# Kernel tuning notes

Hardware: AMD Instinct MI355X
Metric: run time of the kernel (lower is better)

The kernel has to match this reference:

```python
import jax, jax.numpy as jnp
import numpy as np

B, S, N, U, A = 256, 24, 207, 64, 256
H = N * U  # hidden_state_size = num_nodes * rnn_units


def setup_inputs() -> dict:
    key = jax.random.key(0)
    ks = jax.random.split(key, 9)
    return {
        "inputs": jax.random.normal(ks[0], (B, N), dtype=jnp.float32),
        "encoder_outputs": jax.random.normal(ks[1], (S, B, H), dtype=jnp.float32),
        "hidden_state": jax.random.normal(ks[2], (1, B, H), dtype=jnp.float32) * 0.05,
        "adj": jax.random.uniform(ks[3], (N, N), dtype=jnp.float32) / N,
        "attn_W": jax.random.normal(ks[4], (2 * H, A), dtype=jnp.float32) * 0.01,
        "attn_b": jnp.zeros((A,), dtype=jnp.float32),
        "attn_v": jax.random.normal(ks[5], (A,), dtype=jnp.float32) * 0.1,
        "W_ru": jax.random.normal(ks[6], (1 + 2 * U, 2 * U), dtype=jnp.float32) * 0.1,
        "b_ru": jnp.zeros((2 * U,), dtype=jnp.float32),
        "W_c": jax.random.normal(ks[7], (1 + 2 * U, U), dtype=jnp.float32) * 0.1,
        "b_c": jnp.zeros((U,), dtype=jnp.float32),
        "proj_W": jax.random.normal(ks[8], (2 * U + 1, 1), dtype=jnp.float32) * 0.1,
        "proj_b": jnp.zeros((1,), dtype=jnp.float32),
    }


def reference(inputs, encoder_outputs, hidden_state, adj, attn_W, attn_b, attn_v,
              W_ru, b_ru, W_c, b_c, proj_W, proj_b):
    b = inputs.shape[0]
    hid = hidden_state[-1]                               # (B, H) top-layer decoder state
    enc = jnp.transpose(encoder_outputs, (1, 0, 2))      # (B, S, H)

    # Bahdanau attention: tanh(Linear(cat(hid, enc))) . v, softmax over src_len.
    # Split the weight so we never materialize the (B, S, 2H) concat.
    Wh, We = attn_W[:H], attn_W[H:]
    energy = jnp.tanh((hid @ Wh)[:, None, :] + jnp.einsum('bsh,ha->bsa', enc, We) + attn_b)
    scores = energy @ attn_v                             # (B, S)
    a = jax.nn.softmax(scores, axis=1)
    weighted = jnp.einsum('bs,bsh->bh', a, enc).reshape(b, N, U)  # (B, N, U)

    # Graph-conv GRU cell (DCRNN-style), single layer.
    x = jnp.concatenate([inputs.reshape(b, N, 1), weighted], axis=-1)  # (B, N, 1+U)
    h = hid.reshape(b, N, U)
    m = jnp.einsum('nm,bmf->bnf', adj, jnp.concatenate([x, h], axis=-1))  # message passing
    ru = jax.nn.sigmoid(m @ W_ru + b_ru)                 # (B, N, 2U)
    r, u = ru[..., :U], ru[..., U:]
    mc = jnp.einsum('nm,bmf->bnf', adj, jnp.concatenate([x, r * h], axis=-1))
    c = jnp.tanh(mc @ W_c + b_c)                         # (B, N, U)
    new_h = u * h + (1.0 - u) * c                        # (B, N, U)

    # Projection: Linear(2U+1 -> 1) on per-node cat(output, weighted, inputs).
    proj_in = jnp.concatenate([new_h, weighted, inputs.reshape(b, N, 1)], axis=-1)
    output = (proj_in @ proj_W + proj_b).reshape(b, N)   # (B, N*output_dim)
    return output, new_h.reshape(1, b, H)
```

## Files before the change

### kernel.cpp

```cpp
#include <hip/hip_runtime.h>
#include <hip/hip_bf16.h>
#include <math.h>

#define B_ 256
#define S_ 24
#define N_ 207
#define U_ 64
#define A_ 256
#define H_ (N_*U_)
#define H2_ (2*H_)
#define BS_ (B_*S_)
#define NF_ 129
#define FP_ 192
#define KP_ 256

typedef __attribute__((ext_vector_type(8))) short bf16x8;
typedef __attribute__((ext_vector_type(4))) float f32x4;

#define GAS __attribute__((address_space(1)))
#define LAS __attribute__((address_space(3)))

static __device__ __forceinline__ void gload16(const __hip_bfloat16* g, void* lds) {
    __builtin_amdgcn_global_load_lds((const GAS uint32_t*)g, (LAS uint32_t*)lds, 16, 0, 0);
}

template<int BM, int BN, int EPI>
__global__ __launch_bounds__(256)
void mfma_gemm(const __hip_bfloat16* __restrict__ A, int lda,
               const __hip_bfloat16* __restrict__ BT, int ldb,
               void* __restrict__ Cv, int ldc,
               int kchunk, int niter,
               const float* __restrict__ ep0,
               const float* __restrict__ ep1,
               const float* __restrict__ ep2)
{
    constexpr int FM = BM / 32, FN = BN / 32;
    __shared__ __align__(128) char smem[(BM + BN) * 128];
    char* As = smem;
    char* Bs = smem + BM * 128;

    const int tid  = threadIdx.x;
    const int lane = tid & 63;
    const int wid  = tid >> 6;
    const int wr   = wid >> 1, wc = wid & 1;

    const int n0 = blockIdx.x * BN;
    const int m0 = blockIdx.y * BM;
    const long k0 = (long)blockIdx.z * kchunk;

    const int qk = lane >> 4;
    const int fr = lane & 15;
    const int sw = (lane & 7) << 4;

    f32x4 acc[FM][FN] = {};

    for (int it = 0; it < niter; ++it) {
        const long kb = k0 + (long)it * 64;
        #pragma unroll
        for (int p = 0; p < BM / 32; ++p) {
            const int chunk = p * 4 + wid;
            const int blk   = chunk * 64 + lane;
            const int r     = blk >> 3;
            const int klog  = ((blk & 7) << 4) ^ ((r & 7) << 4);
            gload16(A + (size_t)(m0 + r) * lda + kb + (klog >> 1), As + chunk * 1024);
        }
        #pragma unroll
        for (int p = 0; p < BN / 32; ++p) {
            const int chunk = p * 4 + wid;
            const int blk   = chunk * 64 + lane;
            const int r     = blk >> 3;
            const int klog  = ((blk & 7) << 4) ^ ((r & 7) << 4);
            gload16(BT + (size_t)(n0 + r) * ldb + kb + (klog >> 1), Bs + chunk * 1024);
        }
        __syncthreads();
        #pragma unroll
        for (int ks = 0; ks < 2; ++ks) {
            const int ko = ks * 64 + qk * 16;
            bf16x8 a[FM], b[FN];
            #pragma unroll
            for (int i = 0; i < FM; ++i)
                a[i] = *(const bf16x8*)(As + (wr * (BM/2) + i * 16 + fr) * 128 + (ko ^ sw));
            #pragma unroll
            for (int j = 0; j < FN; ++j)
                b[j] = *(const bf16x8*)(Bs + (wc * (BN/2) + j * 16 + fr) * 128 + (ko ^ sw));
            #pragma unroll
            for (int i = 0; i < FM; ++i)
                #pragma unroll
                for (int j = 0; j < FN; ++j)
                    acc[i][j] = __builtin_amdgcn_mfma_f32_16x16x32_bf16(a[i], b[j], acc[i][j], 0, 0, 0);
        }
        __syncthreads();
    }

    #pragma unroll
    for (int mi = 0; mi < FM; ++mi)
        #pragma unroll
        for (int ni = 0; ni < FN; ++ni) {
            const int rbase = m0 + wr * (BM/2) + mi * 16 + qk * 4;
            const int col   = n0 + wc * (BN/2) + ni * 16 + fr;
            #pragma unroll
            for (int q = 0; q < 4; ++q) {
                const int row = rbase + q;
                const float v = acc[mi][ni][q];
                if (EPI == 1) {
                    atomicAdd(&((float*)Cv)[(size_t)row * ldc + col], v);
                } else if (EPI == 2) {
                    ((__hip_bfloat16*)Cv)[(size_t)row * ldc + col] = __float2bfloat16(v);
                } else if (EPI == 3) {
                    const int bb = col >> 6, uu = col & 63;
                    ((__hip_bfloat16*)Cv)[((size_t)row * 256 + bb) * FP_ + 65 + uu] = __float2bfloat16(v);
                } else if (EPI == 4) {
                    float sv = v + ep0[col];
                    ((float*)Cv)[(size_t)row * ldc + col] = 1.f / (1.f + expf(-sv));
                } else {
                    const int nn = row >> 8, bb = row & 255;
                    float cg = tanhf(v + ep0[col]);
                    float ug = ep1[(size_t)row * 128 + 64 + col];
                    float hh = ep2[(size_t)bb * H_ + nn * U_ + col];
                    ((float*)Cv)[(size_t)bb * H_ + nn * U_ + col] = ug * hh + (1.f - ug) * cg;
                }
            }
        }
}

__global__ __launch_bounds__(256)
void gemm_enchid(const float* __restrict__ Aenc,
                 const float* __restrict__ Ahid,
                 const __hip_bfloat16* __restrict__ WTBF,
                 float* __restrict__ P, float* __restrict__ T1,
                 int kchunk, int niter)
{
    __shared__ __align__(128) char smem[(64 + 256) * 128];
    char* As = smem;
    char* Bs = smem + 64*128;

    const int tid  = threadIdx.x;
    const int lane = tid & 63;
    const int wid  = tid >> 6;
    const int wr   = wid >> 1, wc = wid & 1;

    const bool isH = (blockIdx.y >= 96);
    const float* A = isH ? Ahid : Aenc;
    const int m0   = (isH ? (blockIdx.y - 96) : blockIdx.y) * 64;
    const __hip_bfloat16* BT = WTBF + (isH ? 0 : H_);
    float* C = isH ? T1 : P;

    const long k0 = (long)blockIdx.z * kchunk;

    const int qk = lane >> 4;
    const int fr = lane & 15;
    const int sw = (lane & 7) << 4;

    f32x4 acc[2][8] = {};

    for (int it = 0; it < niter; ++it) {
        const long kb = k0 + (long)it * 64;
        #pragma unroll
        for (int h = 0; h < 2; ++h) {
            const int c  = h * 256 + tid;
            const int r  = c >> 3;
            const int kc = c & 7;
            const float* src = A + (size_t)(m0 + r) * H_ + kb + kc * 8;
            const float4 x = *(const float4*)(src);
            const float4 y = *(const float4*)(src + 4);
            union { __hip_bfloat16 hh[8]; int4 u; } pk;
            pk.hh[0] = __float2bfloat16(x.x); pk.hh[1] = __float2bfloat16(x.y);
            pk.hh[2] = __float2bfloat16(x.z); pk.hh[3] = __float2bfloat16(x.w);
            pk.hh[4] = __float2bfloat16(y.x); pk.hh[5] = __float2bfloat16(y.y);
            pk.hh[6] = __float2bfloat16(y.z); pk.hh[7] = __float2bfloat16(y.w);
            *(int4*)(As + r * 128 + ((kc << 4) ^ ((r & 7) << 4))) = pk.u;
        }
        #pragma unroll
        for (int p = 0; p < 8; ++p) {
            const int chunk = p * 4 + wid;
            const int blk   = chunk * 64 + lane;
            const int r     = blk >> 3;
            const int klog  = ((blk & 7) << 4) ^ ((r & 7) << 4);
            gload16(BT + (size_t)r * H2_ + kb + (klog >> 1), Bs + chunk * 1024);
        }
        __syncthreads();
        #pragma unroll
        for (int ks = 0; ks < 2; ++ks) {
            const int ko = ks * 64 + qk * 16;
            bf16x8 a[2], b[8];
            #pragma unroll
            for (int i = 0; i < 2; ++i)
                a[i] = *(const bf16x8*)(As + (wr * 32 + i * 16 + fr) * 128 + (ko ^ sw));
            #pragma unroll
            for (int j = 0; j < 8; ++j)
                b[j] = *(const bf16x8*)(Bs + (wc * 128 + j * 16 + fr) * 128 + (ko ^ sw));
            #pragma unroll
            for (int i = 0; i < 2; ++i)
                #pragma unroll
                for (int j = 0; j < 8; ++j)
                    acc[i][j] = __builtin_amdgcn_mfma_f32_16x16x32_bf16(a[i], b[j], acc[i][j], 0, 0, 0);
        }
        __syncthreads();
    }

    #pragma unroll
    for (int mi = 0; mi < 2; ++mi)
        #pragma unroll
        for (int ni = 0; ni < 8; ++ni) {
            const int rbase = m0 + wr * 32 + mi * 16 + qk * 4;
            const int col   = wc * 128 + ni * 16 + fr;
            #pragma unroll
            for (int q = 0; q < 4; ++q)
                atomicAdd(&C[(size_t)(rbase + q) * A_ + col], acc[mi][ni][q]);
        }
}

__global__ __launch_bounds__(256)
void init_kernel(const float* __restrict__ ab, float* __restrict__ T1,
                 float4* __restrict__ P4) {
    int i = blockIdx.x * 256 + threadIdx.x;
    if (blockIdx.x < 256) {
        T1[i] = ab[i & 255];
    } else {
        P4[i - 65536] = make_float4(0.f, 0.f, 0.f, 0.f);
    }
}

__global__ __launch_bounds__(256)
void transpose_cvt_kernel(const float* __restrict__ in, __hip_bfloat16* __restrict__ out) {
    __shared__ float tile[32][33];
    const int h0 = blockIdx.x * 32, a0 = blockIdx.y * 32;
    const int tx = threadIdx.x & 31, ty4 = threadIdx.x >> 5;
    #pragma unroll
    for (int i = 0; i < 4; ++i) {
        int r = ty4 * 4 + i;
        tile[r][tx] = in[(size_t)(h0 + r) * A_ + a0 + tx];
    }
    __syncthreads();
    #pragma unroll
    for (int i = 0; i < 4; ++i) {
        int r = ty4 * 4 + i;
        out[(size_t)(a0 + r) * H2_ + h0 + tx] = __float2bfloat16(tile[tx][r]);
    }
}

__global__ __launch_bounds__(256)
void scores_kernel(const float* __restrict__ P, const float* __restrict__ T1,
                   const float* __restrict__ v, float* __restrict__ SC) {
    int wave = threadIdx.x >> 6, lane = threadIdx.x & 63;
    int q = blockIdx.x * 4 + wave;
    if (q >= BS_) return;
    int b = q & 255;
    float s = 0.f;
    #pragma unroll
    for (int a = lane; a < A_; a += 64) {
        float e = tanhf(P[(size_t)q * A_ + a] + T1[b * A_ + a]);
        s += e * v[a];
    }
    #pragma unroll
    for (int off = 32; off; off >>= 1) s += __shfl_down(s, off, 64);
    if (lane == 0) SC[q] = s;
}

__global__ __launch_bounds__(256)
void weighted_f32_kernel(const float4* __restrict__ E4, const float* __restrict__ SC,
                         float4* __restrict__ WT4) {
    int g = blockIdx.x * 256 + threadIdx.x;
    int b = g / (H_ / 4), c = g % (H_ / 4);
    float sc[S_];
    float mx = -1e30f;
    #pragma unroll
    for (int s = 0; s < S_; ++s) { sc[s] = SC[s * B_ + b]; mx = fmaxf(mx, sc[s]); }
    float sum = 0.f;
    #pragma unroll
    for (int s = 0; s < S_; ++s) { sc[s] = expf(sc[s] - mx); sum += sc[s]; }
    float inv = 1.f / sum;
    float4 acc = make_float4(0.f, 0.f, 0.f, 0.f);
    #pragma unroll
    for (int s = 0; s < S_; ++s) {
        float w = sc[s] * inv;
        float4 ev = E4[(size_t)(s * B_ + b) * (H_ / 4) + c];
        acc.x += w * ev.x; acc.y += w * ev.y;
        acc.z += w * ev.z; acc.w += w * ev.w;
    }
    WT4[(size_t)b * (H_ / 4) + c] = acc;
}

__global__ __launch_bounds__(256)
void catT_prepB_kernel(const float* __restrict__ inp, const float* __restrict__ WT,
                       const float* __restrict__ hid, __hip_bfloat16* __restrict__ CT,
                       const float* __restrict__ adj, const float* __restrict__ Wru,
                       const float* __restrict__ Wc, __hip_bfloat16* __restrict__ ADJ,
                       __hip_bfloat16* __restrict__ WRUT, __hip_bfloat16* __restrict__ WCT) {
    const int tid = threadIdx.x;
    if (blockIdx.y == 4) {
        for (int i = blockIdx.x * 256 + tid; i < 102400; i += 65536) {
            if (i < 65536) {
                int r = i >> 8, c = i & 255;
                ADJ[i] = __float2bfloat16((r < N_ && c < N_) ? adj[r * N_ + c] : 0.f);
            } else if (i < 90112) {
                int idx = i - 65536;
                int j = idx / FP_, f = idx % FP_;
                WRUT[idx] = __float2bfloat16(f < NF_ ? Wru[f * 128 + j] : 0.f);
            } else {
                int idx = i - 90112;
                int j = idx / FP_, f = idx % FP_;
                WCT[idx] = __float2bfloat16(f < NF_ ? Wc[f * 64 + j] : 0.f);
            }
        }
        return;
    }
    __shared__ float ww[64][65];
    __shared__ float wh[64][65];
    __shared__ float wi[64];
    const int b = blockIdx.x;
    const int k0 = blockIdx.y * 64;
    #pragma unroll
    for (int i = 0; i < 16; ++i) {
        int idx = tid + i * 256;
        int kn = idx >> 6, f = idx & 63;
        int k = k0 + kn;
        bool vld = (k < N_);
        ww[kn][f] = vld ? WT [(size_t)b * H_ + k * 64 + f] : 0.f;
        wh[kn][f] = vld ? hid[(size_t)b * H_ + k * 64 + f] : 0.f;
    }
    if (tid < 64) wi[tid] = (k0 + tid < N_) ? inp[b * N_ + k0 + tid] : 0.f;
    __syncthreads();
    #pragma unroll
    for (int i = 0; i < 6; ++i) {
        int cid = tid + i * 256;
        int f = cid >> 3, kk = (cid & 7) * 8;
        union { __hip_bfloat16 h[8]; bf16x8 v; } pk;
        #pragma unroll
        for (int j = 0; j < 8; ++j) {
            float x;
            if (f == 0)        x = wi[kk + j];
            else if (f <= 64)  x = ww[kk + j][f - 1];
            else if (f <= 128) x = wh[kk + j][f - 65];
            else               x = 0.f;
            pk.h[j] = __float2bfloat16(x);
        }
        *(bf16x8*)(CT + ((size_t)b * FP_ + f) * KP_ + k0 + kk) = pk.v;
    }
}

__global__ __launch_bounds__(256)
void rhT_kernel(const float* __restrict__ RU, const float* __restrict__ hid,
                __hip_bfloat16* __restrict__ RT) {
    __shared__ float rh[64][65];
    const int b = blockIdx.x, k0 = blockIdx.y * 64, tid = threadIdx.x;
    #pragma unroll
    for (int i = 0; i < 16; ++i) {
        int idx = tid + i * 256;
        int kn = idx >> 6, u = idx & 63;
        int k = k0 + kn;
        float v = 0.f;
        if (k < N_)
            v = RU[((size_t)k * 256 + b) * 128 + u] * hid[(size_t)b * H_ + k * 64 + u];
        rh[kn][u] = v;
    }
    __syncthreads();
    #pragma unroll
    for (int i = 0; i < 2; ++i) {
        int cid = tid + i * 256;
        int u = cid >> 3, kk = (cid & 7) * 8;
        union { __hip_bfloat16 h[8]; bf16x8 v; } pk;
        #pragma unroll
        for (int j = 0; j < 8; ++j) pk.h[j] = __float2bfloat16(rh[kk + j][u]);
        *(bf16x8*)(RT + ((size_t)b * 64 + u) * KP_ + k0 + kk) = pk.v;
    }
}

__global__ __launch_bounds__(256)
void proj_kernel(const float* __restrict__ newh, const float* __restrict__ WT,
                 const float* __restrict__ inp, const float* __restrict__ pW,
                 const float* __restrict__ pb, float* __restrict__ out0) {
    int wave = threadIdx.x >> 6, lane = threadIdx.x & 63;
    int idx = blockIdx.x * 4 + wave;
    if (idx >= B_ * N_) return;
    int b = idx / N_, n = idx % N_;
    float t = newh[(size_t)b * H_ + n * U_ + lane] * pW[lane]
            + WT  [(size_t)b * H_ + n * U_ + lane] * pW[64 + lane];
    if (lane == 0) t += inp[b * N_ + n] * pW[128] + pb[0];
    #pragma unroll
    for (int off = 32; off; off >>= 1) t += __shfl_down(t, off, 64);
    if (lane == 0) out0[b * N_ + n] = t;
}

extern "C" void kernel_launch(void* const* d_in, const int* in_sizes, int n_in,
                              void* d_out, int out_size, void* d_ws, size_t ws_size,
                              hipStream_t stream) {
    const float* inp    = (const float*)d_in[0];
    const float* enc    = (const float*)d_in[1];
    const float* hid    = (const float*)d_in[2];
    const float* adj    = (const float*)d_in[3];
    const float* attn_W = (const float*)d_in[4];
    const float* attn_b = (const float*)d_in[5];
    const float* attn_v = (const float*)d_in[6];
    const float* W_ru   = (const float*)d_in[7];
    const float* b_ru   = (const float*)d_in[8];
    const float* W_c    = (const float*)d_in[9];
    const float* b_c    = (const float*)d_in[10];
    const float* proj_W = (const float*)d_in[11];
    const float* proj_b = (const float*)d_in[12];

    float* out0 = (float*)d_out;
    float* out2 = out0 + (size_t)B_ * N_;

    float* ws  = (float*)d_ws;
    float* T1  = ws;
    float* P   = T1 + 65536;
    float* SC  = P  + 1572864;
    float* AW  = SC + 6144;
    float* WT  = AW + 6144;
    float* BIG = WT + 3391488;
    __hip_bfloat16* WT_BF  = (__hip_bfloat16*)(BIG + 40697856);
    __hip_bfloat16* CAT_T  = (__hip_bfloat16*)BIG;
    __hip_bfloat16* MB_BF  = (__hip_bfloat16*)(BIG + 6291456);
    __hip_bfloat16* RH_T   = (__hip_bfloat16*)(BIG + 12582912);
    float*          RU     = BIG + 14680064;
    __hip_bfloat16* ADJ_BF = (__hip_bfloat16*)(BIG + 21463040);
    __hip_bfloat16* WRUT   = (__hip_bfloat16*)(BIG + 21495808);
    __hip_bfloat16* WCT    = (__hip_bfloat16*)(BIG + 21508096);

    transpose_cvt_kernel<<<dim3(H2_/32, A_/32), 256, 0, stream>>>(attn_W, WT_BF);
    init_kernel<<<1792, 256, 0, stream>>>(attn_b, T1, (float4*)P);

    gemm_enchid<<<dim3(1,100,9), 256, 0, stream>>>(
        enc, hid, WT_BF, P, T1, 1472, 23);

    scores_kernel<<<BS_/4, 256, 0, stream>>>(P, T1, attn_v, SC);
    weighted_f32_kernel<<<(B_*(H_/4))/256, 256, 0, stream>>>(
        (const float4*)enc, SC, (float4*)WT);

    catT_prepB_kernel<<<dim3(256,5), 256, 0, stream>>>(
        inp, WT, hid, CAT_T, adj, W_ru, W_c, ADJ_BF, WRUT, WCT);

    mfma_gemm<64,64,2><<<dim3(768,4,1), 256, 0, stream>>>(
        ADJ_BF, KP_, CAT_T, KP_, MB_BF, 49152, 0, 4, nullptr, nullptr, nullptr);

    mfma_gemm<64,64,4><<<dim3(2,828,1), 256, 0, stream>>>(
        MB_BF, FP_, WRUT, FP_, RU, 128, 0, 3, b_ru, nullptr, nullptr);

    rhT_kernel<<<dim3(256,4), 256, 0, stream>>>(RU, hid, RH_T);

    mfma_gemm<64,64,3><<<dim3(256,4,1), 256, 0, stream>>>(
        ADJ_BF, KP_, RH_T, KP_, MB_BF, 0, 0, 4, nullptr, nullptr, nullptr);

    mfma_gemm<64,64,5><<<dim3(1,828,1), 256, 0, stream>>>(
        MB_BF, FP_, WCT, FP_, out2, 0, 0, 3, b_c, RU, hid);

    proj_kernel<<<(B_*N_)/4, 256, 0, stream>>>(out2, WT, inp, proj_W, proj_b, out0);
}
```

Baseline: 307.4 us.

## Fuse projection into GRU epilogue, merge prep kernels, enlarge attention GEMM M-tile

The output projection is folded into the final candidate-gate GEMM epilogue. Per-row dot products are reduced with shuffles and LDS atomics, which removes the separate proj_kernel and its reread of new_h. The weight transpose and the init/zero kernels are merged into one launch. The attention GEMM now uses 128-row tiles instead of 64, halving the passes over the attention weights and the block count, at the cost of more registers and fewer blocks for occupancy.

```diff
diff --git a/kernel.cpp b/kernel.cpp
--- a/kernel.cpp
+++ b/kernel.cpp
@@ -32,7 +32,12 @@
                int kchunk, int niter,
                const float* __restrict__ ep0,
                const float* __restrict__ ep1,
-               const float* __restrict__ ep2)
+               const float* __restrict__ ep2,
+               const float* __restrict__ e_wt,
+               const float* __restrict__ e_pw,
+               const float* __restrict__ e_pb,
+               const float* __restrict__ e_in,
+               float* __restrict__ e_o0)
 {
     constexpr int FM = BM / 32, FN = BN / 32;
     __shared__ __align__(128) char smem[(BM + BN) * 128];
@@ -90,6 +95,19 @@
                     acc[i][j] = __builtin_amdgcn_mfma_f32_16x16x32_bf16(a[i], b[j], acc[i][j], 0, 0, 0);
         }
         __syncthreads();
+    }
+
+    float* rsum = (float*)smem;
+    if (EPI == 5) {
+        if (tid < BM) rsum[tid] = 0.f;
+        __syncthreads();
+    }
+    float tpart[FM][4];
+    if (EPI == 5) {
+        #pragma unroll
+        for (int mi = 0; mi < FM; ++mi)
+            #pragma unroll
+            for (int q = 0; q < 4; ++q) tpart[mi][q] = 0.f;
     }
 
     #pragma unroll
@@ -116,11 +134,34 @@
                     const int nn = row >> 8, bb = row & 255;
                     float cg = tanhf(v + ep0[col]);
                     float ug = ep1[(size_t)row * 128 + 64 + col];
-                    float hh = ep2[(size_t)bb * H_ + nn * U_ + col];
-                    ((float*)Cv)[(size_t)bb * H_ + nn * U_ + col] = ug * hh + (1.f - ug) * cg;
+                    const size_t hoff = (size_t)bb * H_ + nn * U_ + col;
+                    float nh = ug * ep2[hoff] + (1.f - ug) * cg;
+                    ((float*)Cv)[hoff] = nh;
+                    tpart[mi][q] += nh * e_pw[col] + e_wt[hoff] * e_pw[64 + col];
                 }
             }
         }
+
+    if (EPI == 5) {
+        #pragma unroll
+        for (int mi = 0; mi < FM; ++mi)
+            #pragma unroll
+            for (int q = 0; q < 4; ++q) {
+                float t = tpart[mi][q];
+                #pragma unroll
+                for (int off = 8; off; off >>= 1) t += __shfl_xor(t, off, 16);
+                if (fr == 0) {
+                    const int rloc = wr * (BM/2) + mi * 16 + qk * 4 + q;
+                    atomicAdd(&rsum[rloc], t);
+                }
+            }
+        __syncthreads();
+        if (tid < BM) {
+            const int row = m0 + tid;
+            const int nn = row >> 8, bb = row & 255;
+            e_o0[bb * N_ + nn] = rsum[tid] + e_in[bb * N_ + nn] * e_pw[128] + e_pb[0];
+        }
+    }
 }
 
 __global__ __launch_bounds__(256)
@@ -130,18 +171,18 @@
                  float* __restrict__ P, float* __restrict__ T1,
                  int kchunk, int niter)
 {
-    __shared__ __align__(128) char smem[(64 + 256) * 128];
+    __shared__ __align__(128) char smem[(128 + 256) * 128];
     char* As = smem;
-    char* Bs = smem + 64*128;
+    char* Bs = smem + 128*128;
 
     const int tid  = threadIdx.x;
     const int lane = tid & 63;
     const int wid  = tid >> 6;
     const int wr   = wid >> 1, wc = wid & 1;
 
-    const bool isH = (blockIdx.y >= 96);
+    const bool isH = (blockIdx.y >= 48);
     const float* A = isH ? Ahid : Aenc;
-    const int m0   = (isH ? (blockIdx.y - 96) : blockIdx.y) * 64;
+    const int m0   = (isH ? (blockIdx.y - 48) : blockIdx.y) * 128;
     const __hip_bfloat16* BT = WTBF + (isH ? 0 : H_);
     float* C = isH ? T1 : P;
 
@@ -151,12 +192,12 @@
     const int fr = lane & 15;
     const int sw = (lane & 7) << 4;
 
-    f32x4 acc[2][8] = {};
+    f32x4 acc[4][8] = {};
 
     for (int it = 0; it < niter; ++it) {
         const long kb = k0 + (long)it * 64;
         #pragma unroll
-        for (int h = 0; h < 2; ++h) {
+        for (int h = 0; h < 4; ++h) {
             const int c  = h * 256 + tid;
             const int r  = c >> 3;
             const int kc = c & 7;
@@ -182,15 +223,15 @@
         #pragma unroll
         for (int ks = 0; ks < 2; ++ks) {
             const int ko = ks * 64 + qk * 16;
-            bf16x8 a[2], b[8];
-            #pragma unroll
-            for (int i = 0; i < 2; ++i)
-                a[i] = *(const bf16x8*)(As + (wr * 32 + i * 16 + fr) * 128 + (ko ^ sw));
+            bf16x8 a[4], b[8];
+            #pragma unroll
+            for (int i = 0; i < 4; ++i)
+                a[i] = *(const bf16x8*)(As + (wr * 64 + i * 16 + fr) * 128 + (ko ^ sw));
             #pragma unroll
             for (int j = 0; j < 8; ++j)
                 b[j] = *(const bf16x8*)(Bs + (wc * 128 + j * 16 + fr) * 128 + (ko ^ sw));
             #pragma unroll
-            for (int i = 0; i < 2; ++i)
+            for (int i = 0; i < 4; ++i)
                 #pragma unroll
                 for (int j = 0; j < 8; ++j)
                     acc[i][j] = __builtin_amdgcn_mfma_f32_16x16x32_bf16(a[i], b[j], acc[i][j], 0, 0, 0);
@@ -199,10 +240,10 @@
     }
 
     #pragma unroll
-    for (int mi = 0; mi < 2; ++mi)
+    for (int mi = 0; mi < 4; ++mi)
         #pragma unroll
         for (int ni = 0; ni < 8; ++ni) {
-            const int rbase = m0 + wr * 32 + mi * 16 + qk * 4;
+            const int rbase = m0 + wr * 64 + mi * 16 + qk * 4;
             const int col   = wc * 128 + ni * 16 + fr;
             #pragma unroll
             for (int q = 0; q < 4; ++q)
@@ -211,31 +252,30 @@
 }
 
 __global__ __launch_bounds__(256)
-void init_kernel(const float* __restrict__ ab, float* __restrict__ T1,
+void prep_kernel(const float* __restrict__ attnW, __hip_bfloat16* __restrict__ WTBF,
+                 const float* __restrict__ ab, float* __restrict__ T1,
                  float4* __restrict__ P4) {
-    int i = blockIdx.x * 256 + threadIdx.x;
-    if (blockIdx.x < 256) {
-        T1[i] = ab[i & 255];
-    } else {
-        P4[i - 65536] = make_float4(0.f, 0.f, 0.f, 0.f);
-    }
-}
-
-__global__ __launch_bounds__(256)
-void transpose_cvt_kernel(const float* __restrict__ in, __hip_bfloat16* __restrict__ out) {
+    const int tid = threadIdx.x;
+    if (blockIdx.y == 8) {
+        for (int i = blockIdx.x * 256 + tid; i < 458752; i += 828 * 256) {
+            if (i < 65536) T1[i] = ab[i & 255];
+            else           P4[i - 65536] = make_float4(0.f, 0.f, 0.f, 0.f);
+        }
+        return;
+    }
     __shared__ float tile[32][33];
     const int h0 = blockIdx.x * 32, a0 = blockIdx.y * 32;
-    const int tx = threadIdx.x & 31, ty4 = threadIdx.x >> 5;
+    const int tx = tid & 31, ty4 = tid >> 5;
     #pragma unroll
     for (int i = 0; i < 4; ++i) {
         int r = ty4 * 4 + i;
-        tile[r][tx] = in[(size_t)(h0 + r) * A_ + a0 + tx];
+        tile[r][tx] = attnW[(size_t)(h0 + r) * A_ + a0 + tx];
     }
     __syncthreads();
     #pragma unroll
     for (int i = 0; i < 4; ++i) {
         int r = ty4 * 4 + i;
-        out[(size_t)(a0 + r) * H2_ + h0 + tx] = __float2bfloat16(tile[tx][r]);
+        WTBF[(size_t)(a0 + r) * H2_ + h0 + tx] = __float2bfloat16(tile[tx][r]);
     }
 }
 
@@ -366,22 +406,6 @@
     }
 }
 
-__global__ __launch_bounds__(256)
-void proj_kernel(const float* __restrict__ newh, const float* __restrict__ WT,
-                 const float* __restrict__ inp, const float* __restrict__ pW,
-                 const float* __restrict__ pb, float* __restrict__ out0) {
-    int wave = threadIdx.x >> 6, lane = threadIdx.x & 63;
-    int idx = blockIdx.x * 4 + wave;
-    if (idx >= B_ * N_) return;
-    int b = idx / N_, n = idx % N_;
-    float t = newh[(size_t)b * H_ + n * U_ + lane] * pW[lane]
-            + WT  [(size_t)b * H_ + n * U_ + lane] * pW[64 + lane];
-    if (lane == 0) t += inp[b * N_ + n] * pW[128] + pb[0];
-    #pragma unroll
-    for (int off = 32; off; off >>= 1) t += __shfl_down(t, off, 64);
-    if (lane == 0) out0[b * N_ + n] = t;
-}
-
 extern "C" void kernel_launch(void* const* d_in, const int* in_sizes, int n_in,
                               void* d_out, int out_size, void* d_ws, size_t ws_size,
                               hipStream_t stream) {
@@ -418,32 +442,34 @@
     __hip_bfloat16* WRUT   = (__hip_bfloat16*)(BIG + 21495808);
     __hip_bfloat16* WCT    = (__hip_bfloat16*)(BIG + 21508096);
 
-    transpose_cvt_kernel<<<dim3(H2_/32, A_/32), 256, 0, stream>>>(attn_W, WT_BF);
-    init_kernel<<<1792, 256, 0, stream>>>(attn_b, T1, (float4*)P);
-
-    gemm_enchid<<<dim3(1,100,9), 256, 0, stream>>>(
+    prep_kernel<<<dim3(H2_/32, 9), 256, 0, stream>>>(
+        attn_W, WT_BF, attn_b, T1, (float4*)P);
+
+    gemm_enchid<<<dim3(1, 50, 9), 256, 0, stream>>>(
         enc, hid, WT_BF, P, T1, 1472, 23);
 
     scores_kernel<<<BS_/4, 256, 0, stream>>>(P, T1, attn_v, SC);
     weighted_f32_kernel<<<(B_*(H_/4))/256, 256, 0, stream>>>(
         (const float4*)enc, SC, (float4*)WT);
 
-    catT_prepB_kernel<<<dim3(256,5), 256, 0, stream>>>(
+    catT_prepB_kernel<<<dim3(256, 5), 256, 0, stream>>>(
         inp, WT, hid, CAT_T, adj, W_ru, W_c, ADJ_BF, WRUT, WCT);
 
     mfma_gemm<64,64,2><<<dim3(768,4,1), 256, 0, stream>>>(
-        ADJ_BF, KP_, CAT_T, KP_, MB_BF, 49152, 0, 4, nullptr, nullptr, nullptr);
+        ADJ_BF, KP_, CAT_T, KP_, MB_BF, 49152, 0, 4,
+        nullptr, nullptr, nullptr, nullptr, nullptr, nullptr, nullptr, nullptr);
 
     mfma_gemm<64,64,4><<<dim3(2,828,1), 256, 0, stream>>>(
-        MB_BF, FP_, WRUT, FP_, RU, 128, 0, 3, b_ru, nullptr, nullptr);
+        MB_BF, FP_, WRUT, FP_, RU, 128, 0, 3,
+        b_ru, nullptr, nullptr, nullptr, nullptr, nullptr, nullptr, nullptr);
 
     rhT_kernel<<<dim3(256,4), 256, 0, stream>>>(RU, hid, RH_T);
 
     mfma_gemm<64,64,3><<<dim3(256,4,1), 256, 0, stream>>>(
-        ADJ_BF, KP_, RH_T, KP_, MB_BF, 0, 0, 4, nullptr, nullptr, nullptr);
+        ADJ_BF, KP_, RH_T, KP_, MB_BF, 0, 0, 4,
+        nullptr, nullptr, nullptr, nullptr, nullptr, nullptr, nullptr, nullptr);
 
     mfma_gemm<64,64,5><<<dim3(1,828,1), 256, 0, stream>>>(
-        MB_BF, FP_, WCT, FP_, out2, 0, 0, 3, b_c, RU, hid);
-
-    proj_kernel<<<(B_*N_)/4, 256, 0, stream>>>(out2, WT, inp, proj_W, proj_b, out0);
-}
+        MB_BF, FP_, WCT, FP_, out2, 0, 0, 3,
+        b_c, RU, hid, WT, proj_W, proj_b, inp, out0);
+}
```

After: 325.4 us. 1.06x slower.
